# Optimization experiments

Measured on AMD Instinct MI355X. Metric: run time of the kernel, lower is better.

The kernel has to match this reference:

```python
import jax, jax.numpy as jnp
import numpy as np

N_HEAD = 12


def setup_inputs() -> dict:
    key = jax.random.key(0)
    ks = jax.random.split(key, 16)
    B, N, D, P, H = 1, 512, 384, 128, N_HEAD
    s = 0.02
    return {
        'x1d': jax.random.normal(ks[0], (B, N, D), jnp.float32),
        'x2d': jax.random.normal(ks[1], (B, N, N, P), jnp.float32),
        'pose_t': jax.random.normal(ks[2], (B, N, 3), jnp.float32),
        'pose_r': jax.random.normal(ks[3], (B, N, 3, 3), jnp.float32),
        'bias': jnp.zeros((B, 1, N, N), jnp.float32),
        'w_sq': jax.random.normal(ks[4], (D, D), jnp.float32) * s,
        'w_sk': jax.random.normal(ks[5], (D, D), jnp.float32) * s,
        'w_sv': jax.random.normal(ks[6], (D, D), jnp.float32) * s,
        'w_pb': jax.random.normal(ks[7], (P, H), jnp.float32) * s,
        'w_pq': jax.random.normal(ks[8], (D, H * 3 * 4), jnp.float32) * s,
        'w_pk': jax.random.normal(ks[9], (D, H * 3 * 4), jnp.float32) * s,
        'w_pv': jax.random.normal(ks[10], (D, H * 3 * 8), jnp.float32) * s,
        'tpw': jax.random.uniform(ks[11], (H,), jnp.float32),
        'w_pairv': jax.random.normal(ks[12], (P, D), jnp.float32) * s,
        'w_out': jax.random.normal(ks[13], (2 * D + H * 8 * 4, D), jnp.float32) * s,
        'b_out': jnp.zeros((D,), jnp.float32),
    }


def reference(x1d, x2d, pose_t, pose_r, bias, w_sq, w_sk, w_sv, w_pb,
              w_pq, w_pk, w_pv, tpw, w_pairv, w_out, b_out):
    B, N, D = x1d.shape
    H = N_HEAD
    dk = D // H
    scalar_w = 1.0 / np.sqrt(3 * dk)
    point_w_c = 1.0 / np.sqrt(3 * 4 * 9 / 2)
    pair_w = 1.0 / np.sqrt(3)

    T = pose_t                                # [B,N,3]
    R = jnp.swapaxes(pose_r, -1, -2)          # [B,N,3,3] (pose[1]^T as in torch code)

    # scalar attention
    q_s = (x1d @ w_sq).reshape(B, N, H, dk)
    k_s = (x1d @ w_sk).reshape(B, N, H, dk)
    v_s = (x1d @ w_sv).reshape(B, N, H, dk)
    scalar_attn = jnp.einsum('bihc,bjhc->bhij', q_s * scalar_w, k_s)

    # point attention (global frame)
    def affine(pt):  # R @ pt + T
        return jnp.einsum('bnxy,bnhpy->bnhpx', R, pt) + T[:, :, None, None, :]

    q_p = affine((x1d @ w_pq).reshape(B, N, H, 4, 3))
    k_p = affine((x1d @ w_pk).reshape(B, N, H, 4, 3))
    v_p = affine((x1d @ w_pv).reshape(B, N, H, 8, 3))

    dist = jnp.linalg.norm(q_p[:, :, None] - k_p[:, None], axis=-1)  # [B,I,J,H,P]
    pw = point_w_c * jax.nn.softplus(tpw)                            # [H]
    point_attn = -0.5 * pw[:, None, None] * jnp.transpose(dist.sum(-1), (0, 3, 1, 2))

    # pair bias attention
    pair_attn = pair_w * jnp.transpose(x2d @ w_pb, (0, 3, 1, 2))     # [B,H,I,J]

    attn = jax.nn.softmax(scalar_attn + point_attn + pair_attn + bias, axis=-1)

    # aggregations
    out_scalar = jnp.einsum('bhij,bjhc->bihc', attn, v_s).reshape(B, N, D)

    out_pg = jnp.einsum('bhij,bjhcp->bihcp', attn, v_p)              # [B,I,H,8,3]
    # inverse affine: R^T @ (x - T)
    out_pl = jnp.einsum('bnyx,bnhpy->bnhpx', R, out_pg - T[:, :, None, None, :])
    out_pn = jnp.linalg.norm(out_pl, axis=-1).reshape(B, N, H * 8)
    out_pl = out_pl.reshape(B, N, H * 8 * 3)

    v_pair = (x2d @ w_pairv).reshape(B, N, N, H, dk)
    out_pair = jnp.einsum('bhij,bijhc->bihc', attn, v_pair).reshape(B, N, D)

    feat = jnp.concatenate([out_scalar, out_pl, out_pair, out_pn], axis=-1)
    return feat @ w_out + b_out
```

## Files before the change

### kernel.cpp

```cpp
#include <hip/hip_runtime.h>
#include <hip/hip_bf16.h>
#include <math.h>

#define N_  512
#define D_  384
#define H_  12
#define DK_ 32
#define P_  128

typedef short short8 __attribute__((ext_vector_type(8)));
typedef float f32x4  __attribute__((ext_vector_type(4)));

static __device__ __forceinline__ unsigned short f2bf(float f) {
    union { float f; unsigned int u; } v; v.f = f;
    unsigned int r = (v.u + 0x7FFFu + ((v.u >> 16) & 1u)) >> 16;
    return (unsigned short)r;
}
static __device__ __forceinline__ float bf2f(unsigned short u) {
    union { unsigned int u; float f; } v; v.u = ((unsigned int)u) << 16;
    return v.f;
}
static __device__ __forceinline__ short2 pk2bf(float a, float b) {
    __hip_bfloat162 h = __float22bfloat162_rn(make_float2(a, b));
    return *(short2*)&h;
}
typedef union { short8 v; short2 h2[4]; } s8u;

__global__ __launch_bounds__(256, 4) void k_pair(
    const float* __restrict__ x2d, const float* __restrict__ w_pb,
    float* __restrict__ pairlog)
{
    const int t    = threadIdx.x;
    const int wid  = t >> 6;
    const int lane = t & 63;
    const int quad = lane >> 4;
    const int col  = lane & 15;
    const float pair_w = 0.57735027f;

    short8 bfr[4];
    #pragma unroll
    for (int kt = 0; kt < 4; ++kt) {
        #pragma unroll
        for (int jj = 0; jj < 8; ++jj) {
            int p = kt * 32 + quad * 8 + jj;
            bfr[kt][jj] = (col < 12) ? (short)f2bf(w_pb[p * 12 + col]) : (short)0;
        }
    }

    float4 xv[2][8];
    #pragma unroll
    for (int s = 0; s < 2; ++s) {
        const int T  = blockIdx.x * 8 + wid * 2 + s;
        const float* xrow = x2d + ((size_t)((T >> 5) * N_) + ((T & 31) << 4) + col) * P_;
        #pragma unroll
        for (int kt = 0; kt < 4; ++kt) {
            xv[s][kt * 2 + 0] = *(const float4*)(xrow + kt * 32 + quad * 8);
            xv[s][kt * 2 + 1] = *(const float4*)(xrow + kt * 32 + quad * 8 + 4);
        }
    }

    #pragma unroll
    for (int s = 0; s < 2; ++s) {
        const int T  = blockIdx.x * 8 + wid * 2 + s;
        const int i  = T >> 5;
        const int j0 = (T & 31) << 4;
        f32x4 acc = {0.f, 0.f, 0.f, 0.f};
        #pragma unroll
        for (int kt = 0; kt < 4; ++kt) {
            float4 f0 = xv[s][kt * 2 + 0];
            float4 f1 = xv[s][kt * 2 + 1];
            s8u afr;
            afr.h2[0] = pk2bf(f0.x, f0.y);
            afr.h2[1] = pk2bf(f0.z, f0.w);
            afr.h2[2] = pk2bf(f1.x, f1.y);
            afr.h2[3] = pk2bf(f1.z, f1.w);
            acc = __builtin_amdgcn_mfma_f32_16x16x32_bf16(afr.v, bfr[kt], acc, 0, 0, 0);
        }
        if (col < 12) {
            #pragma unroll
            for (int r = 0; r < 4; ++r) {
                int j = j0 + quad * 4 + r;
                pairlog[((size_t)(col * N_ + i)) * N_ + j] = pair_w * acc[r];
            }
        }
    }
}

__global__ __launch_bounds__(384) void k_proj(
    const float* __restrict__ x1d, const float* __restrict__ pose_t,
    const float* __restrict__ pose_r,
    const float* __restrict__ w_sq, const float* __restrict__ w_sk,
    const float* __restrict__ w_sv, const float* __restrict__ w_pq,
    const float* __restrict__ w_pk, const float* __restrict__ w_pv,
    float* __restrict__ qs, float* __restrict__ kst,
    float* __restrict__ qp, float* __restrict__ kpt,
    unsigned short* __restrict__ vcatT)
{
    const int seg = blockIdx.y;
    const int i0  = blockIdx.x * 8;
    const int t   = threadIdx.x;

    __shared__ float raw[8][288];
    __shared__ float Rsh[8][9];
    __shared__ float Tsh[8][3];

    if (seg < 3) {
        const float* __restrict__ w = (seg == 0) ? w_sq : (seg == 1) ? w_sk : w_sv;
        float acc[8];
        #pragma unroll
        for (int r = 0; r < 8; ++r) acc[r] = 0.f;
        for (int d = 0; d < D_; d += 4) {
            float4 xr[8];
            #pragma unroll
            for (int r = 0; r < 8; ++r)
                xr[r] = *(const float4*)(x1d + (i0 + r) * D_ + d);
            #pragma unroll
            for (int e = 0; e < 4; ++e) {
                float wv = w[(d + e) * D_ + t];
                #pragma unroll
                for (int r = 0; r < 8; ++r)
                    acc[r] += ((const float*)&xr[r])[e] * wv;
            }
        }
        if (seg == 0) {
            #pragma unroll
            for (int r = 0; r < 8; ++r) qs[(i0 + r) * D_ + t] = acc[r];
        } else if (seg == 1) {
            *(float4*)(kst + t * N_ + i0)     = make_float4(acc[0], acc[1], acc[2], acc[3]);
            *(float4*)(kst + t * N_ + i0 + 4) = make_float4(acc[4], acc[5], acc[6], acc[7]);
        } else {
            int h = t >> 5, c = t & 31;
            s8u sv;
            #pragma unroll
            for (int r = 0; r < 4; ++r) sv.h2[r] = pk2bf(acc[2*r], acc[2*r+1]);
            *(short8*)(vcatT + ((size_t)h * 64 + c) * N_ + i0) = sv.v;
        }
    } else {
        if (t < 72) Rsh[t / 9][t % 9] = pose_r[(i0 + t / 9) * 9 + t % 9];
        else if (t < 96) {
            int r = (t - 72) / 3, c = (t - 72) % 3;
            Tsh[r][c] = pose_t[(i0 + r) * 3 + c];
        }

        if (t < 288) {
            const float* __restrict__ w;
            int col, ldw;
            if (seg == 3) {
                if (t < 144) { w = w_pq; col = t;       ldw = 144; }
                else         { w = w_pk; col = t - 144; ldw = 144; }
            } else         { w = w_pv; col = t;       ldw = 288; }
            float acc[8];
            #pragma unroll
            for (int r = 0; r < 8; ++r) acc[r] = 0.f;
            for (int d = 0; d < D_; d += 4) {
                float4 xr[8];
                #pragma unroll
                for (int r = 0; r < 8; ++r)
                    xr[r] = *(const float4*)(x1d + (i0 + r) * D_ + d);
                #pragma unroll
                for (int e = 0; e < 4; ++e) {
                    float wv = w[(d + e) * ldw + col];
                    #pragma unroll
                    for (int r = 0; r < 8; ++r)
                        acc[r] += ((const float*)&xr[r])[e] * wv;
                }
            }
            #pragma unroll
            for (int r = 0; r < 8; ++r) raw[r][t] = acc[r];
        }
        __syncthreads();

        if (t < 288) {
            const int x3   = t % 3;
            const int base = t - x3;
            if (seg == 3) {
                const int c = (t < 144) ? t : t - 144;
                if (t < 144) {
                    #pragma unroll
                    for (int r = 0; r < 8; ++r) {
                        float g = Rsh[r][0 + x3] * raw[r][base]
                                + Rsh[r][3 + x3] * raw[r][base + 1]
                                + Rsh[r][6 + x3] * raw[r][base + 2] + Tsh[r][x3];
                        qp[(i0 + r) * 144 + c] = g;
                    }
                } else {
                    float g[8];
                    #pragma unroll
                    for (int r = 0; r < 8; ++r)
                        g[r] = Rsh[r][0 + x3] * raw[r][base]
                             + Rsh[r][3 + x3] * raw[r][base + 1]
                             + Rsh[r][6 + x3] * raw[r][base + 2] + Tsh[r][x3];
                    *(float4*)(kpt + c * N_ + i0)     = make_float4(g[0], g[1], g[2], g[3]);
                    *(float4*)(kpt + c * N_ + i0 + 4) = make_float4(g[4], g[5], g[6], g[7]);
                }
            } else {
                int h = t / 24, pc = t % 24;
                float g[8];
                #pragma unroll
                for (int r = 0; r < 8; ++r)
                    g[r] = Rsh[r][0 + x3] * raw[r][base]
                         + Rsh[r][3 + x3] * raw[r][base + 1]
                         + Rsh[r][6 + x3] * raw[r][base + 2] + Tsh[r][x3];
                s8u sv;
                #pragma unroll
                for (int r = 0; r < 4; ++r) sv.h2[r] = pk2bf(g[2*r], g[2*r+1]);
                *(short8*)(vcatT + ((size_t)h * 64 + 32 + pc) * N_ + i0) = sv.v;
            }
        }
    }
}

__global__ __launch_bounds__(256) void k_sp_soft(
    const float* __restrict__ qs, const float* __restrict__ kst,
    const float* __restrict__ qp, const float* __restrict__ kpt,
    const float* __restrict__ bias, const float* __restrict__ tpw,
    const float* __restrict__ pairlog,
    unsigned short* __restrict__ attn_bf)
{
    const int h  = blockIdx.x / 128;
    const int i0 = (blockIdx.x % 128) * 4;
    const int t  = threadIdx.x;
    const int lane = t & 63;
    const int wid  = t >> 6;
    __shared__ float qsh[4][32];
    __shared__ float qph[4][12];
    __shared__ float wredm[4][4];
    __shared__ float wreds[4][4];
    if (t < 128) { int il = t / 32, c = t % 32; qsh[il][c] = qs[(i0+il) * D_ + h*32 + c]; }
    else if (t < 176) { int r = t - 128; int il = r / 12, c = r % 12; qph[il][c] = qp[(i0+il)*144 + h*12 + c]; }
    const float pwh = 0.13608276f * log1pf(expf(tpw[h]));
    const float scalar_w = 0.10206207f;
    __syncthreads();

    float v[4][2];
    for (int jh = 0; jh < 2; ++jh) {
        int j = t + jh * 256;
        float kv[32];
        #pragma unroll
        for (int c = 0; c < 32; ++c) kv[c] = kst[(h*32 + c) * N_ + j];
        float kp[12];
        #pragma unroll
        for (int c = 0; c < 12; ++c) kp[c] = kpt[(h*12 + c) * N_ + j];

        #pragma unroll
        for (int il = 0; il < 4; ++il) {
            float s = 0.f;
            #pragma unroll
            for (int c = 0; c < 32; ++c) s += qsh[il][c] * kv[c];
            float dsum = 0.f;
            #pragma unroll
            for (int p = 0; p < 4; ++p) {
                float dx = qph[il][p*3+0] - kp[p*3+0];
                float dy = qph[il][p*3+1] - kp[p*3+1];
                float dz = qph[il][p*3+2] - kp[p*3+2];
                dsum += sqrtf(dx*dx + dy*dy + dz*dz);
            }
            v[il][jh] = scalar_w * s - 0.5f * pwh * dsum
                      + bias[(i0+il) * N_ + j]
                      + pairlog[((size_t)(h * N_ + (i0+il))) * N_ + j];
        }
    }

    #pragma unroll
    for (int il = 0; il < 4; ++il) {
        float mt = fmaxf(v[il][0], v[il][1]);
        #pragma unroll
        for (int off = 1; off < 64; off <<= 1)
            mt = fmaxf(mt, __shfl_xor(mt, off));
        if (lane == 0) wredm[il][wid] = mt;
    }
    __syncthreads();
    float m[4];
    #pragma unroll
    for (int il = 0; il < 4; ++il)
        m[il] = fmaxf(fmaxf(wredm[il][0], wredm[il][1]),
                      fmaxf(wredm[il][2], wredm[il][3]));

    #pragma unroll
    for (int il = 0; il < 4; ++il) {
        float e0 = __expf(v[il][0] - m[il]);
        float e1 = __expf(v[il][1] - m[il]);
        v[il][0] = e0; v[il][1] = e1;
        float st = e0 + e1;
        #pragma unroll
        for (int off = 1; off < 64; off <<= 1)
            st += __shfl_xor(st, off);
        if (lane == 0) wreds[il][wid] = st;
    }
    __syncthreads();
    #pragma unroll
    for (int il = 0; il < 4; ++il) {
        float inv = 1.0f / (wreds[il][0] + wreds[il][1] + wreds[il][2] + wreds[il][3]);
        size_t base = ((size_t)(h * N_ + i0 + il)) * N_;
        attn_bf[base + t]       = f2bf(v[il][0] * inv);
        attn_bf[base + t + 256] = f2bf(v[il][1] * inv);
    }
}

__global__ __launch_bounds__(256) void k_mid(
    const unsigned short* __restrict__ attn_bf,
    const float* __restrict__ x2d,
    const unsigned short* __restrict__ vcatT,
    float* __restrict__ tmp,
    float* __restrict__ feat, float* __restrict__ outpg)
{
    __shared__ float4 at[3][N_];
    __shared__ float red[4][1536];

    const int t = threadIdx.x;

    if (blockIdx.x < 512) {
        const int i = blockIdx.x;
        for (int idx = t; idx < 12 * N_; idx += 256) {
            int h = idx >> 9, j = idx & 511;
            float a = bf2f(attn_bf[((size_t)(h * N_ + i)) * N_ + j]);
            ((float*)&at[h >> 2][j])[h & 3] = a;
        }
        __syncthreads();

        const int p2 = (t & 63) * 2;
        const int jh = t >> 6;
        float acc[12][2];
        #pragma unroll
        for (int h = 0; h < 12; ++h) { acc[h][0] = 0.f; acc[h][1] = 0.f; }
        const float* xb = x2d + (size_t)i * N_ * P_ + p2;

        for (int j = jh; j < N_; j += 32) {
            float2 x[8];
            #pragma unroll
            for (int u = 0; u < 8; ++u)
                x[u] = *(const float2*)(xb + (j + u * 4) * P_);
            #pragma unroll
            for (int u = 0; u < 8; ++u) {
                int jj = j + u * 4;
                float4 a0 = at[0][jj], a1 = at[1][jj], a2 = at[2][jj];
                float xx = x[u].x, xy = x[u].y;
                acc[0][0]  += a0.x*xx; acc[0][1]  += a0.x*xy;
                acc[1][0]  += a0.y*xx; acc[1][1]  += a0.y*xy;
                acc[2][0]  += a0.z*xx; acc[2][1]  += a0.z*xy;
                acc[3][0]  += a0.w*xx; acc[3][1]  += a0.w*xy;
                acc[4][0]  += a1.x*xx; acc[4][1]  += a1.x*xy;
                acc[5][0]  += a1.y*xx; acc[5][1]  += a1.y*xy;
                acc[6][0]  += a1.z*xx; acc[6][1]  += a1.z*xy;
                acc[7][0]  += a1.w*xx; acc[7][1]  += a1.w*xy;
                acc[8][0]  += a2.x*xx; acc[8][1]  += a2.x*xy;
                acc[9][0]  += a2.y*xx; acc[9][1]  += a2.y*xy;
                acc[10][0] += a2.z*xx; acc[10][1] += a2.z*xy;
                acc[11][0] += a2.w*xx; acc[11][1] += a2.w*xy;
            }
        }
        #pragma unroll
        for (int h = 0; h < 12; ++h) {
            red[jh][h * 128 + p2]     = acc[h][0];
            red[jh][h * 128 + p2 + 1] = acc[h][1];
        }
        __syncthreads();
        for (int idx = t; idx < 1536; idx += 256)
            tmp[(size_t)i * 1536 + idx] = red[0][idx] + red[1][idx] + red[2][idx] + red[3][idx];
        return;
    }

    const int bid  = blockIdx.x - 512;
    const int h    = bid >> 5;
    const int i0   = (bid & 31) << 4;
    const int wid  = t >> 6;
    const int lane = t & 63;
    const int quad = lane >> 4;
    const int col  = lane & 15;
    const int c    = wid * 16 + col;
    const bool cvalid = (c < 56);

    const unsigned short* arow = attn_bf + ((size_t)(h * N_ + i0 + col)) * N_;
    const unsigned short* brow = vcatT + ((size_t)h * 64 + c) * N_;

    f32x4 acc = {0.f, 0.f, 0.f, 0.f};
    #pragma unroll
    for (int kt = 0; kt < 16; ++kt) {
        const int k0 = kt * 32 + quad * 8;
        short8 a = *(const short8*)(arow + k0);
        short8 b;
        if (cvalid) b = *(const short8*)(brow + k0);
        else { b[0]=0;b[1]=0;b[2]=0;b[3]=0;b[4]=0;b[5]=0;b[6]=0;b[7]=0; }
        acc = __builtin_amdgcn_mfma_f32_16x16x32_bf16(a, b, acc, 0, 0, 0);
    }
    #pragma unroll
    for (int r = 0; r < 4; ++r) {
        int i = i0 + quad * 4 + r;
        if (c < 32)       feat[(size_t)i * 1152 + h * 32 + c] = acc[r];
        else if (c < 56)  outpg[((size_t)i * 12 + h) * 24 + (c - 32)] = acc[r];
    }
}

__global__ __launch_bounds__(384) void k_feat(
    const float* __restrict__ tmp, const float* __restrict__ outpg,
    const float* __restrict__ pose_t, const float* __restrict__ pose_r,
    const float* __restrict__ w_pairv, float* __restrict__ feat)
{
    const int i = blockIdx.x;
    const int t = threadIdx.x;
    __shared__ float tsh[1536];
    __shared__ float pg[288];
    __shared__ float pl[288];
    __shared__ float Rsh[9], Tsh[3];

    for (int idx = t; idx < 1536; idx += 384) tsh[idx] = tmp[(size_t)i * 1536 + idx];
    if (t < 288) pg[t] = outpg[i * 288 + t];
    if (t < 9) Rsh[t] = pose_r[i * 9 + t];
    if (t < 3) Tsh[t] = pose_t[i * 3 + t];
    __syncthreads();

    {
        int h = t >> 5;
        const float* ts = tsh + h * 128;
        float acc = 0.f;
        #pragma unroll 4
        for (int p = 0; p < 128; ++p) acc += ts[p] * w_pairv[p * D_ + t];
        feat[(size_t)i * 1152 + 672 + t] = acc;
    }
    if (t < 288) {
        int x3 = t % 3, base = t - x3;
        float g0 = pg[base + 0] - Tsh[0];
        float g1 = pg[base + 1] - Tsh[1];
        float g2 = pg[base + 2] - Tsh[2];
        float v = Rsh[x3*3+0]*g0 + Rsh[x3*3+1]*g1 + Rsh[x3*3+2]*g2;
        pl[t] = v;
        feat[(size_t)i * 1152 + 384 + t] = v;
    }
    __syncthreads();
    if (t < 96) {
        float a = pl[t*3], b = pl[t*3+1], c = pl[t*3+2];
        feat[(size_t)i * 1152 + 1056 + t] = sqrtf(a*a + b*b + c*c);
    }
}

__global__ __launch_bounds__(384) void k_out_part(
    const float* __restrict__ feat, const float* __restrict__ w_out,
    float* __restrict__ part)
{
    const int kc = blockIdx.x >> 6;
    const int i0 = (blockIdx.x & 63) * 8;
    const int t  = threadIdx.x;
    const int k0 = kc * 144;

    float acc[8];
    #pragma unroll
    for (int r = 0; r < 8; ++r) acc[r] = 0.f;

    for (int d = 0; d < 144; d += 4) {
        float4 fr[8];
        #pragma unroll
        for (int r = 0; r < 8; ++r)
            fr[r] = *(const float4*)(feat + (size_t)(i0 + r) * 1152 + k0 + d);
        #pragma unroll
        for (int e = 0; e < 4; ++e) {
            float wv = w_out[(size_t)(k0 + d + e) * D_ + t];
            #pragma unroll
            for (int r = 0; r < 8; ++r)
                acc[r] += ((const float*)&fr[r])[e] * wv;
        }
    }
    #pragma unroll
    for (int r = 0; r < 8; ++r)
        part[((size_t)kc * N_ + i0 + r) * D_ + t] = acc[r];
}

__global__ __launch_bounds__(256) void k_out_red(
    const float* __restrict__ part, const float* __restrict__ b_out,
    float* __restrict__ out)
{
    const int idx = blockIdx.x * 256 + threadIdx.x;
    float s = b_out[idx % D_];
    #pragma unroll
    for (int kc = 0; kc < 8; ++kc) s += part[(size_t)kc * (N_ * D_) + idx];
    out[idx] = s;
}

extern "C" void kernel_launch(void* const* d_in, const int* in_sizes, int n_in,
                              void* d_out, int out_size, void* d_ws, size_t ws_size,
                              hipStream_t stream)
{
    (void)in_sizes; (void)n_in; (void)out_size; (void)ws_size;
    const float* x1d     = (const float*)d_in[0];
    const float* x2d     = (const float*)d_in[1];
    const float* pose_t  = (const float*)d_in[2];
    const float* pose_r  = (const float*)d_in[3];
    const float* bias    = (const float*)d_in[4];
    const float* w_sq    = (const float*)d_in[5];
    const float* w_sk    = (const float*)d_in[6];
    const float* w_sv    = (const float*)d_in[7];
    const float* w_pb    = (const float*)d_in[8];
    const float* w_pq    = (const float*)d_in[9];
    const float* w_pk    = (const float*)d_in[10];
    const float* w_pv    = (const float*)d_in[11];
    const float* tpw     = (const float*)d_in[12];
    const float* w_pairv = (const float*)d_in[13];
    const float* w_out   = (const float*)d_in[14];
    const float* b_out   = (const float*)d_in[15];
    float* out = (float*)d_out;

    float* ws = (float*)d_ws;
    float* qs      = ws;
    float* kst     = qs      + 196608;
    float* qp      = kst     + 196608;
    float* kpt     = qp      + 73728;
    float* pairlog = kpt     + 73728;
    float* tmp     = pairlog + 3145728;
    float* outpg   = tmp     + 786432;
    float* feat    = outpg   + 147456;
    float* part    = feat    + 589824;
    unsigned short* attn_bf = (unsigned short*)(part + 1572864);
    unsigned short* vcatT   = attn_bf + (size_t)12 * N_ * N_;

    hipLaunchKernelGGL(k_pair, dim3(2048), dim3(256), 0, stream,
                       x2d, w_pb, pairlog);
    hipLaunchKernelGGL(k_proj, dim3(64, 5), dim3(384), 0, stream,
                       x1d, pose_t, pose_r, w_sq, w_sk, w_sv, w_pq, w_pk, w_pv,
                       qs, kst, qp, kpt, vcatT);
    hipLaunchKernelGGL(k_sp_soft, dim3(12 * 128), dim3(256), 0, stream,
                       qs, kst, qp, kpt, bias, tpw, pairlog, attn_bf);
    hipLaunchKernelGGL(k_mid, dim3(512 + 384), dim3(256), 0, stream,
                       attn_bf, x2d, vcatT, tmp, feat, outpg);
    hipLaunchKernelGGL(k_feat, dim3(N_), dim3(384), 0, stream,
                       tmp, outpg, pose_t, pose_r, w_pairv, feat);
    hipLaunchKernelGGL(k_out_part, dim3(512), dim3(384), 0, stream,
                       feat, w_out, part);
    hipLaunchKernelGGL(k_out_red, dim3(768), dim3(256), 0, stream,
                       part, b_out, out);
}
```

Before: 381.2 us.

## Fuse attention-value MFMA into softmax kernel using LDS-staged attention rows

The softmax kernel now processes 16 query rows per block instead of 4, stages the bf16 attention rows in shared memory, and runs the MFMA product against the scalar and point value matrices directly from that LDS tile, writing feat and outpg. The x2d pair aggregation moves into its own kernel (k_tmp), which reads attn_bf from global memory. This removes the global re-read of attention for the MFMA path and one grid segment of the old mixed kernel. In exchange, the grid shrinks to 384 blocks, and v[16][2] plus the 16-row loops raise register pressure and may lower occupancy in the score computation.

```diff
diff --git a/kernel.cpp b/kernel.cpp
--- a/kernel.cpp
+++ b/kernel.cpp
@@ -214,25 +214,32 @@
     const float* __restrict__ qs, const float* __restrict__ kst,
     const float* __restrict__ qp, const float* __restrict__ kpt,
     const float* __restrict__ bias, const float* __restrict__ tpw,
-    const float* __restrict__ pairlog,
-    unsigned short* __restrict__ attn_bf)
-{
-    const int h  = blockIdx.x / 128;
-    const int i0 = (blockIdx.x % 128) * 4;
-    const int t  = threadIdx.x;
+    const float* __restrict__ pairlog, const unsigned short* __restrict__ vcatT,
+    unsigned short* __restrict__ attn_bf,
+    float* __restrict__ feat, float* __restrict__ outpg)
+{
+    const int h  = blockIdx.x >> 5;
+    const int i0 = (blockIdx.x & 31) << 4;
+    const int t    = threadIdx.x;
     const int lane = t & 63;
     const int wid  = t >> 6;
-    __shared__ float qsh[4][32];
-    __shared__ float qph[4][12];
-    __shared__ float wredm[4][4];
-    __shared__ float wreds[4][4];
-    if (t < 128) { int il = t / 32, c = t % 32; qsh[il][c] = qs[(i0+il) * D_ + h*32 + c]; }
-    else if (t < 176) { int r = t - 128; int il = r / 12, c = r % 12; qph[il][c] = qp[(i0+il)*144 + h*12 + c]; }
+
+    __shared__ float qsh[16][32];
+    __shared__ float qph[16][12];
+    __shared__ unsigned short at16[16][520];
+    __shared__ float wredm[16][4];
+    __shared__ float wreds[16][4];
+
+    for (int idx = t; idx < 512; idx += 256) {
+        int il = idx >> 5, c = idx & 31;
+        qsh[il][c] = qs[(i0 + il) * D_ + h * 32 + c];
+    }
+    if (t < 192) { int il = t / 12, c = t % 12; qph[il][c] = qp[(i0+il)*144 + h*12 + c]; }
     const float pwh = 0.13608276f * log1pf(expf(tpw[h]));
     const float scalar_w = 0.10206207f;
     __syncthreads();
 
-    float v[4][2];
+    float v[16][2];
     for (int jh = 0; jh < 2; ++jh) {
         int j = t + jh * 256;
         float kv[32];
@@ -243,7 +250,7 @@
         for (int c = 0; c < 12; ++c) kp[c] = kpt[(h*12 + c) * N_ + j];
 
         #pragma unroll
-        for (int il = 0; il < 4; ++il) {
+        for (int il = 0; il < 16; ++il) {
             float s = 0.f;
             #pragma unroll
             for (int c = 0; c < 32; ++c) s += qsh[il][c] * kv[c];
@@ -262,7 +269,7 @@
     }
 
     #pragma unroll
-    for (int il = 0; il < 4; ++il) {
+    for (int il = 0; il < 16; ++il) {
         float mt = fmaxf(v[il][0], v[il][1]);
         #pragma unroll
         for (int off = 1; off < 64; off <<= 1)
@@ -270,16 +277,12 @@
         if (lane == 0) wredm[il][wid] = mt;
     }
     __syncthreads();
-    float m[4];
-    #pragma unroll
-    for (int il = 0; il < 4; ++il)
-        m[il] = fmaxf(fmaxf(wredm[il][0], wredm[il][1]),
-                      fmaxf(wredm[il][2], wredm[il][3]));
-
-    #pragma unroll
-    for (int il = 0; il < 4; ++il) {
-        float e0 = __expf(v[il][0] - m[il]);
-        float e1 = __expf(v[il][1] - m[il]);
+    #pragma unroll
+    for (int il = 0; il < 16; ++il) {
+        float m = fmaxf(fmaxf(wredm[il][0], wredm[il][1]),
+                        fmaxf(wredm[il][2], wredm[il][3]));
+        float e0 = __expf(v[il][0] - m);
+        float e1 = __expf(v[il][1] - m);
         v[il][0] = e0; v[il][1] = e1;
         float st = e0 + e1;
         #pragma unroll
@@ -289,95 +292,30 @@
     }
     __syncthreads();
     #pragma unroll
-    for (int il = 0; il < 4; ++il) {
+    for (int il = 0; il < 16; ++il) {
         float inv = 1.0f / (wreds[il][0] + wreds[il][1] + wreds[il][2] + wreds[il][3]);
-        size_t base = ((size_t)(h * N_ + i0 + il)) * N_;
-        attn_bf[base + t]       = f2bf(v[il][0] * inv);
-        attn_bf[base + t + 256] = f2bf(v[il][1] * inv);
-    }
-}
-
-__global__ __launch_bounds__(256) void k_mid(
-    const unsigned short* __restrict__ attn_bf,
-    const float* __restrict__ x2d,
-    const unsigned short* __restrict__ vcatT,
-    float* __restrict__ tmp,
-    float* __restrict__ feat, float* __restrict__ outpg)
-{
-    __shared__ float4 at[3][N_];
-    __shared__ float red[4][1536];
-
-    const int t = threadIdx.x;
-
-    if (blockIdx.x < 512) {
-        const int i = blockIdx.x;
-        for (int idx = t; idx < 12 * N_; idx += 256) {
-            int h = idx >> 9, j = idx & 511;
-            float a = bf2f(attn_bf[((size_t)(h * N_ + i)) * N_ + j]);
-            ((float*)&at[h >> 2][j])[h & 3] = a;
-        }
-        __syncthreads();
-
-        const int p2 = (t & 63) * 2;
-        const int jh = t >> 6;
-        float acc[12][2];
-        #pragma unroll
-        for (int h = 0; h < 12; ++h) { acc[h][0] = 0.f; acc[h][1] = 0.f; }
-        const float* xb = x2d + (size_t)i * N_ * P_ + p2;
-
-        for (int j = jh; j < N_; j += 32) {
-            float2 x[8];
-            #pragma unroll
-            for (int u = 0; u < 8; ++u)
-                x[u] = *(const float2*)(xb + (j + u * 4) * P_);
-            #pragma unroll
-            for (int u = 0; u < 8; ++u) {
-                int jj = j + u * 4;
-                float4 a0 = at[0][jj], a1 = at[1][jj], a2 = at[2][jj];
-                float xx = x[u].x, xy = x[u].y;
-                acc[0][0]  += a0.x*xx; acc[0][1]  += a0.x*xy;
-                acc[1][0]  += a0.y*xx; acc[1][1]  += a0.y*xy;
-                acc[2][0]  += a0.z*xx; acc[2][1]  += a0.z*xy;
-                acc[3][0]  += a0.w*xx; acc[3][1]  += a0.w*xy;
-                acc[4][0]  += a1.x*xx; acc[4][1]  += a1.x*xy;
-                acc[5][0]  += a1.y*xx; acc[5][1]  += a1.y*xy;
-                acc[6][0]  += a1.z*xx; acc[6][1]  += a1.z*xy;
-                acc[7][0]  += a1.w*xx; acc[7][1]  += a1.w*xy;
-                acc[8][0]  += a2.x*xx; acc[8][1]  += a2.x*xy;
-                acc[9][0]  += a2.y*xx; acc[9][1]  += a2.y*xy;
-                acc[10][0] += a2.z*xx; acc[10][1] += a2.z*xy;
-                acc[11][0] += a2.w*xx; acc[11][1] += a2.w*xy;
-            }
-        }
-        #pragma unroll
-        for (int h = 0; h < 12; ++h) {
-            red[jh][h * 128 + p2]     = acc[h][0];
-            red[jh][h * 128 + p2 + 1] = acc[h][1];
-        }
-        __syncthreads();
-        for (int idx = t; idx < 1536; idx += 256)
-            tmp[(size_t)i * 1536 + idx] = red[0][idx] + red[1][idx] + red[2][idx] + red[3][idx];
-        return;
-    }
-
-    const int bid  = blockIdx.x - 512;
-    const int h    = bid >> 5;
-    const int i0   = (bid & 31) << 4;
-    const int wid  = t >> 6;
-    const int lane = t & 63;
+        at16[il][t]       = f2bf(v[il][0] * inv);
+        at16[il][t + 256] = f2bf(v[il][1] * inv);
+    }
+    __syncthreads();
+
+    for (int idx = t; idx < 16 * 64; idx += 256) {
+        int row = idx >> 6, seg = idx & 63;
+        short8 a = *(const short8*)&at16[row][seg * 8];
+        *(short8*)(attn_bf + ((size_t)(h * N_ + i0 + row)) * N_ + seg * 8) = a;
+    }
+
     const int quad = lane >> 4;
     const int col  = lane & 15;
     const int c    = wid * 16 + col;
     const bool cvalid = (c < 56);
-
-    const unsigned short* arow = attn_bf + ((size_t)(h * N_ + i0 + col)) * N_;
     const unsigned short* brow = vcatT + ((size_t)h * 64 + c) * N_;
 
     f32x4 acc = {0.f, 0.f, 0.f, 0.f};
     #pragma unroll
     for (int kt = 0; kt < 16; ++kt) {
         const int k0 = kt * 32 + quad * 8;
-        short8 a = *(const short8*)(arow + k0);
+        short8 a = *(const short8*)&at16[col][k0];
         short8 b;
         if (cvalid) b = *(const short8*)(brow + k0);
         else { b[0]=0;b[1]=0;b[2]=0;b[3]=0;b[4]=0;b[5]=0;b[6]=0;b[7]=0; }
@@ -389,6 +327,65 @@
         if (c < 32)       feat[(size_t)i * 1152 + h * 32 + c] = acc[r];
         else if (c < 56)  outpg[((size_t)i * 12 + h) * 24 + (c - 32)] = acc[r];
     }
+}
+
+__global__ __launch_bounds__(256) void k_tmp(
+    const unsigned short* __restrict__ attn_bf,
+    const float* __restrict__ x2d,
+    float* __restrict__ tmp)
+{
+    __shared__ float4 at[3][N_];
+    __shared__ float red[4][1536];
+
+    const int t = threadIdx.x;
+    const int i = blockIdx.x;
+
+    for (int idx = t; idx < 12 * N_; idx += 256) {
+        int h = idx >> 9, j = idx & 511;
+        float a = bf2f(attn_bf[((size_t)(h * N_ + i)) * N_ + j]);
+        ((float*)&at[h >> 2][j])[h & 3] = a;
+    }
+    __syncthreads();
+
+    const int p2 = (t & 63) * 2;
+    const int jh = t >> 6;
+    float acc[12][2];
+    #pragma unroll
+    for (int h = 0; h < 12; ++h) { acc[h][0] = 0.f; acc[h][1] = 0.f; }
+    const float* xb = x2d + (size_t)i * N_ * P_ + p2;
+
+    for (int j = jh; j < N_; j += 32) {
+        float2 x[8];
+        #pragma unroll
+        for (int u = 0; u < 8; ++u)
+            x[u] = *(const float2*)(xb + (j + u * 4) * P_);
+        #pragma unroll
+        for (int u = 0; u < 8; ++u) {
+            int jj = j + u * 4;
+            float4 a0 = at[0][jj], a1 = at[1][jj], a2 = at[2][jj];
+            float xx = x[u].x, xy = x[u].y;
+            acc[0][0]  += a0.x*xx; acc[0][1]  += a0.x*xy;
+            acc[1][0]  += a0.y*xx; acc[1][1]  += a0.y*xy;
+            acc[2][0]  += a0.z*xx; acc[2][1]  += a0.z*xy;
+            acc[3][0]  += a0.w*xx; acc[3][1]  += a0.w*xy;
+            acc[4][0]  += a1.x*xx; acc[4][1]  += a1.x*xy;
+            acc[5][0]  += a1.y*xx; acc[5][1]  += a1.y*xy;
+            acc[6][0]  += a1.z*xx; acc[6][1]  += a1.z*xy;
+            acc[7][0]  += a1.w*xx; acc[7][1]  += a1.w*xy;
+            acc[8][0]  += a2.x*xx; acc[8][1]  += a2.x*xy;
+            acc[9][0]  += a2.y*xx; acc[9][1]  += a2.y*xy;
+            acc[10][0] += a2.z*xx; acc[10][1] += a2.z*xy;
+            acc[11][0] += a2.w*xx; acc[11][1] += a2.w*xy;
+        }
+    }
+    #pragma unroll
+    for (int h = 0; h < 12; ++h) {
+        red[jh][h * 128 + p2]     = acc[h][0];
+        red[jh][h * 128 + p2 + 1] = acc[h][1];
+    }
+    __syncthreads();
+    for (int idx = t; idx < 1536; idx += 256)
+        tmp[(size_t)i * 1536 + idx] = red[0][idx] + red[1][idx] + red[2][idx] + red[3][idx];
 }
 
 __global__ __launch_bounds__(384) void k_feat(
@@ -516,10 +513,11 @@
     hipLaunchKernelGGL(k_proj, dim3(64, 5), dim3(384), 0, stream,
                        x1d, pose_t, pose_r, w_sq, w_sk, w_sv, w_pq, w_pk, w_pv,
                        qs, kst, qp, kpt, vcatT);
-    hipLaunchKernelGGL(k_sp_soft, dim3(12 * 128), dim3(256), 0, stream,
-                       qs, kst, qp, kpt, bias, tpw, pairlog, attn_bf);
-    hipLaunchKernelGGL(k_mid, dim3(512 + 384), dim3(256), 0, stream,
-                       attn_bf, x2d, vcatT, tmp, feat, outpg);
+    hipLaunchKernelGGL(k_sp_soft, dim3(12 * 32), dim3(256), 0, stream,
+                       qs, kst, qp, kpt, bias, tpw, pairlog, vcatT,
+                       attn_bf, feat, outpg);
+    hipLaunchKernelGGL(k_tmp, dim3(N_), dim3(256), 0, stream,
+                       attn_bf, x2d, tmp);
     hipLaunchKernelGGL(k_feat, dim3(N_), dim3(384), 0, stream,
                        tmp, outpg, pose_t, pose_r, w_pairv, feat);
     hipLaunchKernelGGL(k_out_part, dim3(512), dim3(384), 0, stream,
```

Result: slower. 448.9 us (+17.8%).
